# Kernel tuning notes

Measured on AMD Instinct MI355X. Metric: run time of the kernel, lower is better.

The kernel has to match this reference:

```python
import jax, jax.numpy as jnp
import numpy as np

B_, K_, D_, L_, N_, R_ = 4, 4, 96, 2048, 16, 6
C_ = R_ + 2 * N_  # 38


def setup_inputs() -> dict:
    key = jax.random.key(0)
    ks = jax.random.split(key, 6)
    scale = 0.05  # keep projections in a realistic range (like 1/sqrt(fan_in) init)
    return {
        "xs": jax.random.normal(ks[0], (B_, K_, D_, L_), dtype=jnp.float32),
        "A_logs": jax.random.uniform(ks[1], (K_ * D_, N_), dtype=jnp.float32),
        "Ds": jax.random.normal(ks[2], (K_ * D_,), dtype=jnp.float32),
        "dt_projs_weight": jax.random.normal(ks[3], (K_, D_, R_), dtype=jnp.float32) * scale,
        "dt_projs_bias": jax.random.normal(ks[4], (K_, D_), dtype=jnp.float32) * scale,
        "x_proj_weight": jax.random.normal(ks[5], (K_, C_, D_), dtype=jnp.float32) * scale,
    }


def reference(xs, A_logs, Ds, dt_projs_weight, dt_projs_bias, x_proj_weight):
    B, K, D, L = xs.shape
    N = A_logs.shape[1]
    R = dt_projs_weight.shape[2]

    xs = xs.astype(jnp.float32)  # force_fp32=True

    # project x -> (delta, B, C):  [B,K,C,L]
    x_dbl = jnp.einsum("bkdl,kcd->bkcl", xs, x_proj_weight)
    dts, Bs, Cs = x_dbl[:, :, :R], x_dbl[:, :, R:R + N], x_dbl[:, :, R + N:]
    # dt low-rank -> per-channel delta: [B,K,D,L]
    dts = jnp.einsum("bkrl,kdr->bkdl", dts, dt_projs_weight)

    A = -jnp.exp(A_logs.astype(jnp.float32)).reshape(K, D, N)  # [K,D,N]
    Dskd = Ds.astype(jnp.float32).reshape(K, D)

    # delta_softplus with delta_bias
    delta = jax.nn.softplus(dts + dt_projs_bias.astype(jnp.float32)[None, :, :, None])

    # discretization: deltaA [B,K,D,L,N], deltaB_u [B,K,D,L,N]
    dA = jnp.exp(delta[..., None] * A[None, :, :, None, :])
    dBu = jnp.einsum("bkdl,bknl,bkdl->bkdln", delta, Bs, xs)

    # linear recurrence h_t = dA_t * h_{t-1} + dBu_t via parallel associative scan over L
    def combine(e1, e2):
        a1, b1 = e1
        a2, b2 = e2
        return a1 * a2, a2 * b1 + b2

    _, hs = jax.lax.associative_scan(combine, (dA, dBu), axis=3)  # hs: [B,K,D,L,N]

    # y_t = C_t . h_t + D * x_t
    y = jnp.einsum("bkdln,bknl->bkdl", hs, Cs) + Dskd[None, :, :, None] * xs
    return y.astype(jnp.float32)  # [B,K,D,L]
```

## Files before the change

kernel.cpp:

```cpp
#include <hip/hip_runtime.h>
#include <hip/hip_fp16.h>
#include <math.h>

#define B_ 4
#define K_ 4
#define D_ 96
#define L_ 2048
#define N_ 16
#define R_ 6
#define C_ 38
#define CH 16
#define TPR 128

__device__ __forceinline__ float softplus_f(float x) {
    return fmaxf(x, 0.f) + __logf(1.f + __expf(-fabsf(x)));
}

#if __has_builtin(__builtin_amdgcn_exp2f)
__device__ __forceinline__ float exp2_fast(float x) { return __builtin_amdgcn_exp2f(x); }
#else
__device__ __forceinline__ float exp2_fast(float x) { return __expf(0.6931471805599453f * x); }
#endif

__device__ __forceinline__ float h2f(const uint4& v, int e) {
    return __half2float(((const __half*)&v)[e]);
}


__global__ __launch_bounds__(256) void proj_kernel(
    const float* __restrict__ xs, const float* __restrict__ xpw,
    uint4* __restrict__ BCc, float* __restrict__ dts_ws)
{
    __shared__ float sWt[D_][8];
    const int bk = blockIdx.x;
    const int k = bk & 3;
    const int cg = blockIdx.z;
    const int tid = threadIdx.x;

    int c0, nr;
    if (cg < 4)       { c0 = R_ + cg * 8; nr = 8; }
    else if (cg == 4) { c0 = 0;           nr = 4; }
    else              { c0 = 4;           nr = 2; }

    for (int i = tid; i < 8 * D_; i += 256) {
        const int r = i / D_, dd = i % D_;
        sWt[dd][r] = (r < nr) ? xpw[(k * C_ + c0 + r) * D_ + dd] : 0.f;
    }
    __syncthreads();

    const int l = blockIdx.y * 256 + tid;
    const float* Xl = xs + (size_t)bk * D_ * L_ + l;

    float acc[8];
#pragma unroll
    for (int r = 0; r < 8; ++r) acc[r] = 0.f;

#pragma unroll
    for (int d = 0; d < D_; ++d) {
        const float xv = Xl[d * L_];
        float4 w0 = *(const float4*)&sWt[d][0];
        float4 w1 = *(const float4*)&sWt[d][4];
        acc[0] = fmaf(w0.x, xv, acc[0]); acc[1] = fmaf(w0.y, xv, acc[1]);
        acc[2] = fmaf(w0.z, xv, acc[2]); acc[3] = fmaf(w0.w, xv, acc[3]);
        acc[4] = fmaf(w1.x, xv, acc[4]); acc[5] = fmaf(w1.y, xv, acc[5]);
        acc[6] = fmaf(w1.z, xv, acc[6]); acc[7] = fmaf(w1.w, xv, acc[7]);
    }

    if (cg < 4) {
        const int i8 = l & 15, t8 = l >> 4;
        union { __half h[8]; uint4 v; } p;
#pragma unroll
        for (int e = 0; e < 8; ++e) p.h[e] = __float2half(acc[e]);
        BCc[(((size_t)bk * 16 + i8) * 4 + cg) * TPR + t8] = p.v;
    } else {
        const int rbase = (cg == 4) ? 0 : 4;
        const int rcnt = (cg == 4) ? 4 : 2;
        for (int r = 0; r < rcnt; ++r)
            dts_ws[((size_t)bk * R_ + rbase + r) * L_ + l] = acc[r];
    }
}

__global__ __launch_bounds__(256) void scan_kernel(
    const float* __restrict__ xs, const float* __restrict__ A_logs,
    const float* __restrict__ Ds, const float* __restrict__ dtw,
    const float* __restrict__ dtb, const float* __restrict__ dts_ws,
    const uint4* __restrict__ BCc, float* __restrict__ out)
{
    __shared__ float sAw[4][8];
    __shared__ float sBw[4][8];
    __shared__ float sy[TPR][17];

    const int bkd = blockIdx.x;
    const int d = bkd % D_;
    const int bk = bkd / D_;
    const int k = bk & 3;
    const int kd = k * D_ + d;
    const int tid = threadIdx.x;
    const int g = tid >> 7;
    const int t = tid & (TPR - 1);
    const int lane = tid & 63;
    const int gw = tid >> 6;

    const uint4* BC = BCc + (size_t)bk * 16 * 4 * TPR;
    const int jB = g, jC = 2 + g;

    const float4* xv4 = (const float4*)(xs + (size_t)bkd * L_);
    float x[CH];
#pragma unroll
    for (int q = 0; q < 4; ++q)
        *(float4*)&x[q * 4] = xv4[t * 4 + q];

    float del[CH];
    const float bias = dtb[kd];
#pragma unroll
    for (int j = 0; j < CH; ++j) del[j] = bias;
    const float* w2 = dtw + (size_t)kd * R_;
    const float4* dts4 = (const float4*)(dts_ws + (size_t)bk * R_ * L_);
#pragma unroll
    for (int r = 0; r < R_; ++r) {
        const float wr = w2[r];
#pragma unroll
        for (int q = 0; q < 4; ++q) {
            const float4 tv = dts4[r * (L_ / 4) + t * 4 + q];
            del[q * 4 + 0] = fmaf(wr, tv.x, del[q * 4 + 0]);
            del[q * 4 + 1] = fmaf(wr, tv.y, del[q * 4 + 1]);
            del[q * 4 + 2] = fmaf(wr, tv.z, del[q * 4 + 2]);
            del[q * 4 + 3] = fmaf(wr, tv.w, del[q * 4 + 3]);
        }
    }
#pragma unroll
    for (int j = 0; j < CH; ++j) del[j] = softplus_f(del[j]);

    float A2[8];
    const float* Ap = A_logs + (size_t)kd * N_ + g * 8;
#pragma unroll
    for (int n = 0; n < 8; ++n) A2[n] = -__expf(Ap[n]) * 1.44269504f;
    const float Dval = Ds[kd];

    float a[8], b[8];
#pragma unroll
    for (int n = 0; n < 8; ++n) { a[n] = 1.f; b[n] = 0.f; }
#pragma unroll
    for (int i = 0; i < CH; ++i) {
        const uint4 cB = BC[(i * 4 + jB) * TPR + t];
        const float dl = del[i];
        const float dx = dl * x[i];
#pragma unroll
        for (int n = 0; n < 8; ++n) {
            const float dA = exp2_fast(dl * A2[n]);
            b[n] = fmaf(dA, b[n], dx * h2f(cB, n));
            a[n] *= dA;
        }
    }

#pragma unroll
    for (int off = 1; off < 64; off <<= 1) {
#pragma unroll
        for (int n = 0; n < 8; ++n) {
            const float pa = __shfl_up(a[n], off, 64);
            const float pb = __shfl_up(b[n], off, 64);
            if (lane >= off) {
                b[n] = fmaf(a[n], pb, b[n]);
                a[n] *= pa;
            }
        }
    }
    if (lane == 63) {
#pragma unroll
        for (int n = 0; n < 8; ++n) { sAw[gw][n] = a[n]; sBw[gw][n] = b[n]; }
    }
    __syncthreads();

    float h[8];
#pragma unroll
    for (int n = 0; n < 8; ++n) {
        float ae = __shfl_up(a[n], 1, 64);
        float be = __shfl_up(b[n], 1, 64);
        if (lane == 0) { ae = 1.f; be = 0.f; }
        float wb = 0.f;
        for (int w = g * 2; w < gw; ++w) wb = fmaf(sAw[w][n], wb, sBw[w][n]);
        h[n] = fmaf(ae, wb, be);
    }

    float yv[CH];
#pragma unroll
    for (int i = 0; i < CH; ++i) {
        const uint4 cB = BC[(i * 4 + jB) * TPR + t];
        const uint4 cC = BC[(i * 4 + jC) * TPR + t];
        const float dl = del[i];
        const float dx = dl * x[i];
        float y = (g == 0) ? Dval * x[i] : 0.f;
#pragma unroll
        for (int n = 0; n < 8; ++n) {
            const float dA = exp2_fast(dl * A2[n]);
            h[n] = fmaf(dA, h[n], dx * h2f(cB, n));
            y = fmaf(h[n], h2f(cC, n), y);
        }
        yv[i] = y;
    }

    if (g == 1) {
#pragma unroll
        for (int j = 0; j < CH; ++j) sy[t][j] = yv[j];
    }
    __syncthreads();
    if (g == 0) {
#pragma unroll
        for (int j = 0; j < CH; ++j) yv[j] += sy[t][j];
        float4* ov = (float4*)(out + (size_t)bkd * L_);
#pragma unroll
        for (int q = 0; q < 4; ++q)
            ov[t * 4 + q] = make_float4(yv[q * 4], yv[q * 4 + 1],
                                        yv[q * 4 + 2], yv[q * 4 + 3]);
    }
}

extern "C" void kernel_launch(void* const* d_in, const int* in_sizes, int n_in,
                              void* d_out, int out_size, void* d_ws, size_t ws_size,
                              hipStream_t stream) {
    const float* xs = (const float*)d_in[0];
    const float* A_logs = (const float*)d_in[1];
    const float* Ds = (const float*)d_in[2];
    const float* dtw = (const float*)d_in[3];
    const float* dtb = (const float*)d_in[4];
    const float* xpw = (const float*)d_in[5];
    float* out = (float*)d_out;

    uint4* BCc = (uint4*)d_ws;
    float* dts_ws = (float*)(BCc + (size_t)B_ * K_ * 16 * 4 * TPR);

    proj_kernel<<<dim3(B_ * K_, 8, 6), 256, 0, stream>>>(xs, xpw, BCc, dts_ws);
    scan_kernel<<<B_ * K_ * D_, 256, 0, stream>>>(
        xs, A_logs, Ds, dtw, dtb, dts_ws, BCc, out);
}
```

Measured before the change: 111.7 us.

## Use one wave per state half in scan, split projection over D halves

The scan kernel now uses 128 threads (one 64-lane wave per half of the N states) with 32 timesteps per lane. The cross-wave carry combine through shared memory and one barrier are removed, leaving a single wave-level shuffle scan. The output is staged in padded shared memory so stores are coalesced. The projection kernel computes 16 channels per thread with the D reduction split across two thread halves, cutting the grid from 6 to 3 channel groups. The cost is longer serial chains per lane and more register pressure from 32-element del/x arrays.

```diff
diff --git a/kernel.cpp b/kernel.cpp
--- a/kernel.cpp
+++ b/kernel.cpp
@@ -9,8 +9,8 @@
 #define N_ 16
 #define R_ 6
 #define C_ 38
-#define CH 16
-#define TPR 128
+#define CH 32
+#define TPR 64
 
 __device__ __forceinline__ float softplus_f(float x) {
     return fmaxf(x, 0.f) + __logf(1.f + __expf(-fabsf(x)));
@@ -31,64 +31,83 @@
     const float* __restrict__ xs, const float* __restrict__ xpw,
     uint4* __restrict__ BCc, float* __restrict__ dts_ws)
 {
-    __shared__ float sWt[D_][8];
+    __shared__ float sWt[2][48][16];
+    __shared__ float sAcc[128][17];
     const int bk = blockIdx.x;
     const int k = bk & 3;
     const int cg = blockIdx.z;
     const int tid = threadIdx.x;
-
-    int c0, nr;
-    if (cg < 4)       { c0 = R_ + cg * 8; nr = 8; }
-    else if (cg == 4) { c0 = 0;           nr = 4; }
-    else              { c0 = 4;           nr = 2; }
-
-    for (int i = tid; i < 8 * D_; i += 256) {
-        const int r = i / D_, dd = i % D_;
-        sWt[dd][r] = (r < nr) ? xpw[(k * C_ + c0 + r) * D_ + dd] : 0.f;
+    const int dh = tid >> 7;
+    const int lt = tid & 127;
+
+    const int c0 = (cg == 0) ? R_ : (cg == 1) ? (R_ + N_) : 0;
+    const int nr = (cg == 2) ? R_ : 16;
+
+    for (int i = tid; i < 2 * 48 * 16; i += 256) {
+        const int hh = i / 768, rem = i % 768, r = rem / 48, dd = rem % 48;
+        sWt[hh][dd][r] = (r < nr) ? xpw[(k * C_ + c0 + r) * D_ + hh * 48 + dd] : 0.f;
     }
     __syncthreads();
 
-    const int l = blockIdx.y * 256 + tid;
-    const float* Xl = xs + (size_t)bk * D_ * L_ + l;
-
-    float acc[8];
-#pragma unroll
-    for (int r = 0; r < 8; ++r) acc[r] = 0.f;
-
-#pragma unroll
-    for (int d = 0; d < D_; ++d) {
-        const float xv = Xl[d * L_];
-        float4 w0 = *(const float4*)&sWt[d][0];
-        float4 w1 = *(const float4*)&sWt[d][4];
-        acc[0] = fmaf(w0.x, xv, acc[0]); acc[1] = fmaf(w0.y, xv, acc[1]);
-        acc[2] = fmaf(w0.z, xv, acc[2]); acc[3] = fmaf(w0.w, xv, acc[3]);
-        acc[4] = fmaf(w1.x, xv, acc[4]); acc[5] = fmaf(w1.y, xv, acc[5]);
-        acc[6] = fmaf(w1.z, xv, acc[6]); acc[7] = fmaf(w1.w, xv, acc[7]);
-    }
-
-    if (cg < 4) {
-        const int i8 = l & 15, t8 = l >> 4;
-        union { __half h[8]; uint4 v; } p;
-#pragma unroll
-        for (int e = 0; e < 8; ++e) p.h[e] = __float2half(acc[e]);
-        BCc[(((size_t)bk * 16 + i8) * 4 + cg) * TPR + t8] = p.v;
-    } else {
-        const int rbase = (cg == 4) ? 0 : 4;
-        const int rcnt = (cg == 4) ? 4 : 2;
-        for (int r = 0; r < rcnt; ++r)
-            dts_ws[((size_t)bk * R_ + rbase + r) * L_ + l] = acc[r];
-    }
-}
-
-__global__ __launch_bounds__(256) void scan_kernel(
+    const int l = blockIdx.y * 128 + lt;
+    const float* Xl = xs + (size_t)bk * D_ * L_ + (size_t)(dh * 48) * L_ + l;
+
+    float acc[16];
+#pragma unroll
+    for (int r = 0; r < 16; ++r) acc[r] = 0.f;
+
+#pragma unroll
+    for (int dd = 0; dd < 48; ++dd) {
+        const float xv = Xl[dd * L_];
+        const float4 w0 = *(const float4*)&sWt[dh][dd][0];
+        const float4 w1 = *(const float4*)&sWt[dh][dd][4];
+        const float4 w2 = *(const float4*)&sWt[dh][dd][8];
+        const float4 w3 = *(const float4*)&sWt[dh][dd][12];
+        acc[0]  = fmaf(w0.x, xv, acc[0]);  acc[1]  = fmaf(w0.y, xv, acc[1]);
+        acc[2]  = fmaf(w0.z, xv, acc[2]);  acc[3]  = fmaf(w0.w, xv, acc[3]);
+        acc[4]  = fmaf(w1.x, xv, acc[4]);  acc[5]  = fmaf(w1.y, xv, acc[5]);
+        acc[6]  = fmaf(w1.z, xv, acc[6]);  acc[7]  = fmaf(w1.w, xv, acc[7]);
+        acc[8]  = fmaf(w2.x, xv, acc[8]);  acc[9]  = fmaf(w2.y, xv, acc[9]);
+        acc[10] = fmaf(w2.z, xv, acc[10]); acc[11] = fmaf(w2.w, xv, acc[11]);
+        acc[12] = fmaf(w3.x, xv, acc[12]); acc[13] = fmaf(w3.y, xv, acc[13]);
+        acc[14] = fmaf(w3.z, xv, acc[14]); acc[15] = fmaf(w3.w, xv, acc[15]);
+    }
+
+    if (dh == 1) {
+#pragma unroll
+        for (int r = 0; r < 16; ++r) sAcc[lt][r] = acc[r];
+    }
+    __syncthreads();
+    if (dh == 0) {
+#pragma unroll
+        for (int r = 0; r < 16; ++r) acc[r] += sAcc[lt][r];
+
+        if (cg < 2) {
+            const int i32 = l & 31, t32 = l >> 5;
+            const int j0 = (cg == 0) ? 0 : 2;
+            union { __half h[8]; uint4 v; } p0, p1;
+#pragma unroll
+            for (int e = 0; e < 8; ++e) {
+                p0.h[e] = __float2half(acc[e]);
+                p1.h[e] = __float2half(acc[8 + e]);
+            }
+            BCc[(((size_t)bk * 32 + i32) * 4 + j0) * TPR + t32] = p0.v;
+            BCc[(((size_t)bk * 32 + i32) * 4 + j0 + 1) * TPR + t32] = p1.v;
+        } else {
+#pragma unroll
+            for (int r = 0; r < R_; ++r)
+                dts_ws[((size_t)bk * R_ + r) * L_ + l] = acc[r];
+        }
+    }
+}
+
+__global__ __launch_bounds__(128) void scan_kernel(
     const float* __restrict__ xs, const float* __restrict__ A_logs,
     const float* __restrict__ Ds, const float* __restrict__ dtw,
     const float* __restrict__ dtb, const float* __restrict__ dts_ws,
     const uint4* __restrict__ BCc, float* __restrict__ out)
 {
-    __shared__ float sAw[4][8];
-    __shared__ float sBw[4][8];
-    __shared__ float sy[TPR][17];
+    __shared__ float sy[2][TPR * 33];
 
     const int bkd = blockIdx.x;
     const int d = bkd % D_;
@@ -96,19 +115,11 @@
     const int k = bk & 3;
     const int kd = k * D_ + d;
     const int tid = threadIdx.x;
-    const int g = tid >> 7;
-    const int t = tid & (TPR - 1);
-    const int lane = tid & 63;
-    const int gw = tid >> 6;
-
-    const uint4* BC = BCc + (size_t)bk * 16 * 4 * TPR;
+    const int g = tid >> 6;
+    const int t = tid & 63;
+
+    const uint4* BC = BCc + (size_t)bk * 32 * 4 * TPR;
     const int jB = g, jC = 2 + g;
-
-    const float4* xv4 = (const float4*)(xs + (size_t)bkd * L_);
-    float x[CH];
-#pragma unroll
-    for (int q = 0; q < 4; ++q)
-        *(float4*)&x[q * 4] = xv4[t * 4 + q];
 
     float del[CH];
     const float bias = dtb[kd];
@@ -120,8 +131,8 @@
     for (int r = 0; r < R_; ++r) {
         const float wr = w2[r];
 #pragma unroll
-        for (int q = 0; q < 4; ++q) {
-            const float4 tv = dts4[r * (L_ / 4) + t * 4 + q];
+        for (int q = 0; q < 8; ++q) {
+            const float4 tv = dts4[r * (L_ / 4) + t * 8 + q];
             del[q * 4 + 0] = fmaf(wr, tv.x, del[q * 4 + 0]);
             del[q * 4 + 1] = fmaf(wr, tv.y, del[q * 4 + 1]);
             del[q * 4 + 2] = fmaf(wr, tv.z, del[q * 4 + 2]);
@@ -137,19 +148,26 @@
     for (int n = 0; n < 8; ++n) A2[n] = -__expf(Ap[n]) * 1.44269504f;
     const float Dval = Ds[kd];
 
+    const float4* xv4 = (const float4*)(xs + (size_t)bkd * L_);
+
     float a[8], b[8];
 #pragma unroll
     for (int n = 0; n < 8; ++n) { a[n] = 1.f; b[n] = 0.f; }
-#pragma unroll
-    for (int i = 0; i < CH; ++i) {
-        const uint4 cB = BC[(i * 4 + jB) * TPR + t];
-        const float dl = del[i];
-        const float dx = dl * x[i];
-#pragma unroll
-        for (int n = 0; n < 8; ++n) {
-            const float dA = exp2_fast(dl * A2[n]);
-            b[n] = fmaf(dA, b[n], dx * h2f(cB, n));
-            a[n] *= dA;
+    {
+        float x[CH];
+#pragma unroll
+        for (int q = 0; q < 8; ++q) *(float4*)&x[q * 4] = xv4[t * 8 + q];
+#pragma unroll
+        for (int i = 0; i < CH; ++i) {
+            const uint4 cB = BC[(i * 4 + jB) * TPR + t];
+            const float dl = del[i];
+            const float dx = dl * x[i];
+#pragma unroll
+            for (int n = 0; n < 8; ++n) {
+                const float dA = exp2_fast(dl * A2[n]);
+                b[n] = fmaf(dA, b[n], dx * h2f(cB, n));
+                a[n] *= dA;
+            }
         }
     }
 
@@ -159,59 +177,48 @@
         for (int n = 0; n < 8; ++n) {
             const float pa = __shfl_up(a[n], off, 64);
             const float pb = __shfl_up(b[n], off, 64);
-            if (lane >= off) {
+            if (t >= off) {
                 b[n] = fmaf(a[n], pb, b[n]);
                 a[n] *= pa;
             }
         }
     }
-    if (lane == 63) {
-#pragma unroll
-        for (int n = 0; n < 8; ++n) { sAw[gw][n] = a[n]; sBw[gw][n] = b[n]; }
+
+    float h[8];
+#pragma unroll
+    for (int n = 0; n < 8; ++n) {
+        const float be = __shfl_up(b[n], 1, 64);
+        h[n] = (t == 0) ? 0.f : be;
+    }
+
+    {
+        float x[CH];
+#pragma unroll
+        for (int q = 0; q < 8; ++q) *(float4*)&x[q * 4] = xv4[t * 8 + q];
+#pragma unroll
+        for (int i = 0; i < CH; ++i) {
+            const uint4 cB = BC[(i * 4 + jB) * TPR + t];
+            const uint4 cC = BC[(i * 4 + jC) * TPR + t];
+            const float dl = del[i];
+            const float dx = dl * x[i];
+            float y = (g == 0) ? Dval * x[i] : 0.f;
+#pragma unroll
+            for (int n = 0; n < 8; ++n) {
+                const float dA = exp2_fast(dl * A2[n]);
+                h[n] = fmaf(dA, h[n], dx * h2f(cB, n));
+                y = fmaf(h[n], h2f(cC, n), y);
+            }
+            sy[g][t * 33 + i] = y;
+        }
     }
     __syncthreads();
 
-    float h[8];
-#pragma unroll
-    for (int n = 0; n < 8; ++n) {
-        float ae = __shfl_up(a[n], 1, 64);
-        float be = __shfl_up(b[n], 1, 64);
-        if (lane == 0) { ae = 1.f; be = 0.f; }
-        float wb = 0.f;
-        for (int w = g * 2; w < gw; ++w) wb = fmaf(sAw[w][n], wb, sBw[w][n]);
-        h[n] = fmaf(ae, wb, be);
-    }
-
-    float yv[CH];
-#pragma unroll
-    for (int i = 0; i < CH; ++i) {
-        const uint4 cB = BC[(i * 4 + jB) * TPR + t];
-        const uint4 cC = BC[(i * 4 + jC) * TPR + t];
-        const float dl = del[i];
-        const float dx = dl * x[i];
-        float y = (g == 0) ? Dval * x[i] : 0.f;
-#pragma unroll
-        for (int n = 0; n < 8; ++n) {
-            const float dA = exp2_fast(dl * A2[n]);
-            h[n] = fmaf(dA, h[n], dx * h2f(cB, n));
-            y = fmaf(h[n], h2f(cC, n), y);
-        }
-        yv[i] = y;
-    }
-
-    if (g == 1) {
-#pragma unroll
-        for (int j = 0; j < CH; ++j) sy[t][j] = yv[j];
-    }
-    __syncthreads();
-    if (g == 0) {
-#pragma unroll
-        for (int j = 0; j < CH; ++j) yv[j] += sy[t][j];
-        float4* ov = (float4*)(out + (size_t)bkd * L_);
-#pragma unroll
-        for (int q = 0; q < 4; ++q)
-            ov[t * 4 + q] = make_float4(yv[q * 4], yv[q * 4 + 1],
-                                        yv[q * 4 + 2], yv[q * 4 + 3]);
+    float* op = out + (size_t)bkd * L_;
+#pragma unroll
+    for (int j = 0; j < 16; ++j) {
+        const int l = j * 128 + tid;
+        const int ti = l >> 5, ii = l & 31;
+        op[l] = sy[0][ti * 33 + ii] + sy[1][ti * 33 + ii];
     }
 }
 
@@ -227,9 +234,9 @@
     float* out = (float*)d_out;
 
     uint4* BCc = (uint4*)d_ws;
-    float* dts_ws = (float*)(BCc + (size_t)B_ * K_ * 16 * 4 * TPR);
-
-    proj_kernel<<<dim3(B_ * K_, 8, 6), 256, 0, stream>>>(xs, xpw, BCc, dts_ws);
-    scan_kernel<<<B_ * K_ * D_, 256, 0, stream>>>(
+    float* dts_ws = (float*)(BCc + (size_t)B_ * K_ * 32 * 4 * TPR);
+
+    proj_kernel<<<dim3(B_ * K_, 16, 3), 256, 0, stream>>>(xs, xpw, BCc, dts_ws);
+    scan_kernel<<<B_ * K_ * D_, 128, 0, stream>>>(
         xs, A_logs, Ds, dtw, dtb, dts_ws, BCc, out);
 }
```

Result: slower. 154.1 us (+38.0%).
